# Kernel optimization log

Measured on AMD Instinct MI355X. Metric: run time of the kernel, lower is better.

## Reference

```python
import jax, jax.numpy as jnp
import numpy as np

BH, BW = 64, 64            # base model input (block) size
STRIDE = 16                # block // 4, per WindowObjectDetector.predict
N_CLASSES = 10
THRESH = 0.7


def _extract_patches(x, bh, bw, stride):
    # x: [1, H, W, 3] -> [R, C, bh, bw, 3], VALID padding (tf.image.extract_patches)
    H, W = x.shape[1], x.shape[2]
    R = (H - bh) // stride + 1
    C = (W - bw) // stride + 1
    r = (jnp.arange(R) * stride)[:, None] + jnp.arange(bh)   # [R, bh]
    c = (jnp.arange(C) * stride)[:, None] + jnp.arange(bw)   # [C, bw]
    p = x[0][r]                 # [R, bh, W, 3]
    p = p[:, :, c]              # [R, bh, C, bw, 3]
    return jnp.transpose(p, (0, 2, 1, 3, 4))  # [R, C, bh, bw, 3]


def _connected_components(mask):
    # mask: bool [K, R, C]; 4-connectivity min-label propagation.
    K, R, C = mask.shape
    BIG = jnp.int32(R * C + 2)
    seed = (jnp.arange(R * C, dtype=jnp.int32).reshape(R, C) + 1)[None]  # [1,R,C]
    lbl0 = jnp.where(mask, seed, 0)

    def prop(l):
        xm = jnp.where(mask, l, BIG)
        n = xm
        n = jnp.minimum(n, jnp.pad(xm, ((0, 0), (1, 0), (0, 0)), constant_values=R * C + 2)[:, :R, :])
        n = jnp.minimum(n, jnp.pad(xm, ((0, 0), (0, 1), (0, 0)), constant_values=R * C + 2)[:, 1:, :])
        n = jnp.minimum(n, jnp.pad(xm, ((0, 0), (0, 0), (1, 0)), constant_values=R * C + 2)[:, :, :C])
        n = jnp.minimum(n, jnp.pad(xm, ((0, 0), (0, 0), (0, 1)), constant_values=R * C + 2)[:, :, 1:])
        return jnp.where(mask, n, 0)

    def cond(carry):
        prev, cur = carry
        return jnp.any(prev != cur)

    def body(carry):
        _, cur = carry
        return cur, prop(cur)

    _, lbl = jax.lax.while_loop(cond, body, (lbl0, prop(lbl0)))
    return lbl  # [K, R, C] int32, 0 = background


def _boxes_from_labels(labels):
    # labels: [K, R, C] -> padded boxes [K, R*C+1, 4] (rowmin-1, colmin-1, rowmax+1, colmax+1)
    K, R, C = labels.shape
    S = R * C + 1
    rr = jnp.repeat(jnp.arange(R, dtype=jnp.int32), C)  # [R*C]
    cc = jnp.tile(jnp.arange(C, dtype=jnp.int32), R)
    flat = labels.reshape(K, R * C)

    def per_class(lbl_k):
        rmin = jax.ops.segment_min(rr, lbl_k, num_segments=S)
        rmax = jax.ops.segment_max(rr, lbl_k, num_segments=S)
        cmin = jax.ops.segment_min(cc, lbl_k, num_segments=S)
        cmax = jax.ops.segment_max(cc, lbl_k, num_segments=S)
        cnt = jax.ops.segment_sum(jnp.ones_like(lbl_k), lbl_k, num_segments=S)
        valid = (cnt > 0) & (jnp.arange(S) > 0)
        box = jnp.stack([rmin - 1, cmin - 1, rmax + 1, cmax + 1], axis=-1)
        box = jnp.where(valid[:, None], box, -1)
        return box, valid

    return jax.vmap(per_class)(flat)


def setup_inputs() -> dict:
    key = jax.random.key(0)
    k1, k2, k3 = jax.random.split(key, 3)
    inputs = jax.random.uniform(k1, (1, 1024, 1024, 3), dtype=jnp.float32)
    W = jax.random.normal(k2, (BH * BW * 3, N_CLASSES), dtype=jnp.float32) * 0.02
    b = jax.random.normal(k3, (N_CLASSES,), dtype=jnp.float32)
    return {"inputs": inputs, "W": W, "b": b}


def reference(inputs, W, b):
    # Windowing: extract 64x64 patches with stride 16 (image divisible by 64 -> no resize)
    patches = _extract_patches(inputs, BH, BW, STRIDE)          # [R, C, 64, 64, 3]
    R, C = patches.shape[0], patches.shape[1]
    flat = patches.reshape(R * C, BH * BW * 3)
    logits = flat @ W + b                                        # base model
    prob = jax.nn.softmax(logits, axis=1).reshape(R, C, N_CLASSES)
    mask = prob > THRESH                                         # [R, C, K]
    # tf transposes before/after connected_components (4-connectivity is symmetric)
    labels = _connected_components(jnp.transpose(mask, (2, 0, 1)))  # [K, R, C]
    labels = jnp.transpose(labels, (1, 2, 0))                    # [R, C, K]
    boxes, valid = _boxes_from_labels(jnp.transpose(labels, (2, 0, 1)))
    return prob, labels, boxes, valid
```

## Files before the change

kernel.cpp:

```cpp
#include <hip/hip_runtime.h>
#include <math.h>

#define RG 61
#define CG 61
#define NP 3721
#define NSEG 3722
#define NCLS 10
#define KTOT 12288
#define NPATCH 8
#define KS 2
#define PAIRS_SLICE 3072
#define ITERS 12
#define THRESHV 0.7f
#define BIGI 0x3FFFFFFF

#define DECLBUF(S) float4 wa##S, wb##S, wc##S, wd##S, we##S; \
                   float2 x0##S, x1##S, x2##S, x3##S, x4##S, x5##S, x6##S, x7##S;

#define LOADW(S, IT) { \
    const int e_   = (ksbase + (IT) * 256 + tid) << 1; \
    const int i_   = e_ / 192; \
    const int rem_ = e_ - i_ * 192; \
    const float* wp_ = W + e_ * NCLS;           \
    wa##S = *(const float4*)(wp_); \
    wb##S = *(const float4*)(wp_ + 4); \
    wc##S = *(const float4*)(wp_ + 8); \
    wd##S = *(const float4*)(wp_ + 12); \
    we##S = *(const float4*)(wp_ + 16); \
    const float* xb_ = imgr + i_ * 3072 + rem_; \
    x0##S = *(const float2*)(xb_); \
    x1##S = *(const float2*)(xb_ + 48); \
    x2##S = *(const float2*)(xb_ + 96); \
    x3##S = *(const float2*)(xb_ + 144); \
    x4##S = *(const float2*)(xb_ + 192); \
    x5##S = *(const float2*)(xb_ + 240); \
    x6##S = *(const float2*)(xb_ + 288); \
    x7##S = *(const float2*)(xb_ + 336); \
}

#define FMAS(S) { \
    const float w0_[NCLS] = {wa##S.x, wa##S.y, wa##S.z, wa##S.w, \
                             wb##S.x, wb##S.y, wb##S.z, wb##S.w, wc##S.x, wc##S.y}; \
    const float w1_[NCLS] = {wc##S.z, wc##S.w, wd##S.x, wd##S.y, \
                             wd##S.z, wd##S.w, we##S.x, we##S.y, we##S.z, we##S.w}; \
    const float2 xs_[NPATCH] = {x0##S, x1##S, x2##S, x3##S, x4##S, x5##S, x6##S, x7##S}; \
    _Pragma("unroll") \
    for (int p_ = 0; p_ < NPATCH; ++p_) { \
        _Pragma("unroll") \
        for (int k_ = 0; k_ < NCLS; ++k_) { \
            acc[p_][k_] = fmaf(xs_[p_].x, w0_[k_], acc[p_][k_]); \
            acc[p_][k_] = fmaf(xs_[p_].y, w1_[k_], acc[p_][k_]); \
        } \
    } \
}

#define SBAR() __builtin_amdgcn_sched_barrier(0)

__global__ __launch_bounds__(256, 2) void wod_logits_part(
    const float* __restrict__ img,
    const float* __restrict__ W,
    float* __restrict__ part)
{
    const int tid = threadIdx.x;
    const int blk = blockIdx.x;
    const int ks  = (blk >= 488) ? 1 : 0;
    const int g   = blk - ks * 488;
    const int r   = g >> 3;
    const int cg  = g & 7;
    const int c0  = (cg < 7) ? cg * 8 : 53;

    const int ksbase = ks * PAIRS_SLICE;
    const float* imgr = img + (16 * r) * 3072 + c0 * 48;

    float acc[NPATCH][NCLS];
    #pragma unroll
    for (int p = 0; p < NPATCH; ++p)
        #pragma unroll
        for (int k = 0; k < NCLS; ++k) acc[p][k] = 0.f;

    DECLBUF(A)
    DECLBUF(B)

    LOADW(A, 0)
    #pragma unroll 1
    for (int t = 0; t < ITERS / 2; ++t) {
        SBAR();
        LOADW(B, 2 * t + 1)
        SBAR();
        FMAS(A)
        SBAR();
        if (t < ITERS / 2 - 1) { LOADW(A, 2 * t + 2) }
        SBAR();
        FMAS(B)
        SBAR();
    }

    #pragma unroll
    for (int p = 0; p < NPATCH; ++p)
        #pragma unroll
        for (int k = 0; k < NCLS; ++k) {
            float v = acc[p][k];
            v += __shfl_down(v, 1);
            v += __shfl_down(v, 2);
            v += __shfl_down(v, 4);
            acc[p][k] = v;
        }

    __shared__ float red[32][81];
    const int lane = tid & 63, wave = tid >> 6;
    if ((lane & 7) == 0) {
        const int row = wave * 8 + (lane >> 3);
        #pragma unroll
        for (int p = 0; p < NPATCH; ++p)
            #pragma unroll
            for (int k = 0; k < NCLS; ++k)
                red[row][p * NCLS + k] = acc[p][k];
    }
    __syncthreads();
    if (tid < NPATCH * NCLS) {
        float s = 0.f;
        #pragma unroll
        for (int j = 0; j < 32; ++j) s += red[j][tid];
        part[blk * (NPATCH * NCLS) + tid] = s;
    }
}

__global__ __launch_bounds__(256) void wod_reduce(
    const float* __restrict__ part,
    const float* __restrict__ bias,
    float* __restrict__ out_prob,
    int* __restrict__ mask)
{
    const int cell = blockIdx.x * 256 + threadIdx.x;
    if (cell >= NP) return;
    const int r  = cell / CG;
    const int c  = cell - r * CG;
    int cg = c >> 3; if (cg > 7) cg = 7;
    const int c0 = (cg < 7) ? cg * 8 : 53;
    const int p  = c - c0;
    const int g  = r * 8 + cg;
    const int gb0 = g * (NPATCH * NCLS) + p * NCLS;
    const int gb1 = (488 + g) * (NPATCH * NCLS) + p * NCLS;

    float lg[NCLS];
    #pragma unroll
    for (int k = 0; k < NCLS; ++k)
        lg[k] = bias[k] + part[gb0 + k] + part[gb1 + k];

    float m = -1e30f;
    #pragma unroll
    for (int k = 0; k < NCLS; ++k) m = fmaxf(m, lg[k]);
    float ex[NCLS], s = 0.f;
    #pragma unroll
    for (int k = 0; k < NCLS; ++k) { ex[k] = expf(lg[k] - m); s += ex[k]; }
    const float inv = 1.f / s;
    const int base = cell * NCLS;
    #pragma unroll
    for (int k = 0; k < NCLS; ++k) {
        const float pr = ex[k] * inv;
        out_prob[base + k] = pr;
        mask[k * NP + cell] = (pr > THRESHV) ? 1 : 0;
    }
}

__global__ __launch_bounds__(256) void wod_cc(
    const int* __restrict__ mask,
    float* __restrict__ out_lbl,
    float* __restrict__ out_box,
    float* __restrict__ out_valid)
{
    const int k = blockIdx.x;
    const int tid = threadIdx.x;
    __shared__ int lbl[NP];
    __shared__ int ext0[NSEG], ext1[NSEG];
    __shared__ int changed;

    const int* mk = mask + k * NP;
    for (int idx = tid; idx < NP; idx += 256)
        lbl[idx] = mk[idx] ? (idx + 1) : 0;
    if (tid == 0) changed = 0;
    __syncthreads();

    for (;;) {
        for (int idx = tid; idx < NP; idx += 256) {
            int v = lbl[idx];
            if (v) {
                const int rr = idx / CG;
                const int cc = idx - rr * CG;
                int best = v;
                if (rr > 0)      { int n = lbl[idx - CG]; if (n && n < best) best = n; }
                if (rr < RG - 1) { int n = lbl[idx + CG]; if (n && n < best) best = n; }
                if (cc > 0)      { int n = lbl[idx - 1];  if (n && n < best) best = n; }
                if (cc < CG - 1) { int n = lbl[idx + 1];  if (n && n < best) best = n; }
                if (best < v) { lbl[idx] = best; changed = 1; }
            }
        }
        __syncthreads();
        const bool stop = (changed == 0);
        __syncthreads();
        if (stop) break;
        if (tid == 0) changed = 0;
        __syncthreads();
    }

    for (int idx = tid; idx < NP; idx += 256)
        out_lbl[idx * NCLS + k] = (float)lbl[idx];

    float* boxk = out_box + k * NSEG * 4;
    float* valk = out_valid + k * NSEG;

    for (int s = tid; s < NSEG; s += 256) { ext0[s] = BIGI; ext1[s] = BIGI; }
    __syncthreads();
    for (int idx = tid; idx < NP; idx += 256) {
        const int v = lbl[idx];
        if (v) {
            const int rr = idx / CG, cc = idx - rr * CG;
            atomicMin(&ext0[v], rr);
            atomicMin(&ext1[v], cc);
        }
    }
    __syncthreads();
    for (int s = tid; s < NSEG; s += 256) {
        const bool valid = (s > 0) && (ext0[s] != BIGI);
        boxk[s * 4 + 0] = valid ? (float)(ext0[s] - 1) : -1.f;
        boxk[s * 4 + 1] = valid ? (float)(ext1[s] - 1) : -1.f;
        valk[s] = valid ? 1.f : 0.f;
    }
    __syncthreads();

    for (int s = tid; s < NSEG; s += 256) { ext0[s] = -1; ext1[s] = -1; }
    __syncthreads();
    for (int idx = tid; idx < NP; idx += 256) {
        const int v = lbl[idx];
        if (v) {
            const int rr = idx / CG, cc = idx - rr * CG;
            atomicMax(&ext0[v], rr);
            atomicMax(&ext1[v], cc);
        }
    }
    __syncthreads();
    for (int s = tid; s < NSEG; s += 256) {
        const bool valid = (s > 0) && (ext0[s] >= 0);
        boxk[s * 4 + 2] = valid ? (float)(ext0[s] + 1) : -1.f;
        boxk[s * 4 + 3] = valid ? (float)(ext1[s] + 1) : -1.f;
    }
}

extern "C" void kernel_launch(void* const* d_in, const int* in_sizes, int n_in,
                              void* d_out, int out_size, void* d_ws, size_t ws_size,
                              hipStream_t stream) {
    (void)in_sizes; (void)n_in; (void)out_size; (void)ws_size;
    const float* img = (const float*)d_in[0];
    const float* W   = (const float*)d_in[1];
    const float* b   = (const float*)d_in[2];

    float* out       = (float*)d_out;
    float* out_prob  = out;
    float* out_lbl   = out + 37210;
    float* out_box   = out + 74420;
    float* out_valid = out + 223300;

    int*   mask = (int*)d_ws;
    float* part = (float*)d_ws + NCLS * NP;

    hipLaunchKernelGGL(wod_logits_part, dim3(KS * 488), dim3(256), 0, stream,
                       img, W, part);
    hipLaunchKernelGGL(wod_reduce, dim3((NP + 255) / 256), dim3(256), 0, stream,
                       part, b, out_prob, mask);
    hipLaunchKernelGGL(wod_cc, dim3(NCLS), dim3(256), 0, stream,
                       mask, out_lbl, out_box, out_valid);
}
```

Baseline: 50.96 us.

## Stage image rows in LDS and retile logits GEMM to four patches per block

Each logits block now copies a 32-row by 336-float slab of the image into shared memory once, then reads patch pixels from LDS instead of global memory. Blocks cover four patches instead of eight, which doubles the block count to 1952, and blocks are remapped in an interleaved order; the launch bound is raised to three blocks per SM. The reduce kernel is updated to the new partial-sum layout. This trades more W reloads across blocks and a 43 KB LDS footprint for better parallelism and lower global-memory traffic on the image.

New measurement: 53.56 us. 5.1% more time.

```diff
diff --git a/kernel.cpp b/kernel.cpp
--- a/kernel.cpp
+++ b/kernel.cpp
@@ -6,36 +6,37 @@
 #define NP 3721
 #define NSEG 3722
 #define NCLS 10
-#define KTOT 12288
-#define NPATCH 8
+#define NPATCH 4
+#define NCG 16
 #define KS 2
-#define PAIRS_SLICE 3072
+#define NBLK (RG*NCG*KS)
+#define ROWS_SLICE 32
 #define ITERS 12
+#define IMGF 336
+#define LDSF (ROWS_SLICE*IMGF)
 #define THRESHV 0.7f
 #define BIGI 0x3FFFFFFF
 
+#define SBAR() __builtin_amdgcn_sched_barrier(0)
+
 #define DECLBUF(S) float4 wa##S, wb##S, wc##S, wd##S, we##S; \
-                   float2 x0##S, x1##S, x2##S, x3##S, x4##S, x5##S, x6##S, x7##S;
-
-#define LOADW(S, IT) { \
-    const int e_   = (ksbase + (IT) * 256 + tid) << 1; \
-    const int i_   = e_ / 192; \
-    const int rem_ = e_ - i_ * 192; \
-    const float* wp_ = W + e_ * NCLS;           \
+                   float2 x0##S, x1##S, x2##S, x3##S;
+
+#define LOADAB(S, IT) { \
+    const int pi_  = (IT) * 256 + tid; \
+    const int il_  = pi_ / 96;                \
+    const int rem_ = (pi_ - il_ * 96) * 2;    \
+    const float* wp_ = W + (size_t)((ks * ROWS_SLICE + il_) * 192 + rem_) * NCLS; \
     wa##S = *(const float4*)(wp_); \
     wb##S = *(const float4*)(wp_ + 4); \
     wc##S = *(const float4*)(wp_ + 8); \
     wd##S = *(const float4*)(wp_ + 12); \
     we##S = *(const float4*)(wp_ + 16); \
-    const float* xb_ = imgr + i_ * 3072 + rem_; \
+    const float* xb_ = s + il_ * IMGF + rem_; \
     x0##S = *(const float2*)(xb_); \
     x1##S = *(const float2*)(xb_ + 48); \
     x2##S = *(const float2*)(xb_ + 96); \
     x3##S = *(const float2*)(xb_ + 144); \
-    x4##S = *(const float2*)(xb_ + 192); \
-    x5##S = *(const float2*)(xb_ + 240); \
-    x6##S = *(const float2*)(xb_ + 288); \
-    x7##S = *(const float2*)(xb_ + 336); \
 }
 
 #define FMAS(S) { \
@@ -43,7 +44,7 @@
                              wb##S.x, wb##S.y, wb##S.z, wb##S.w, wc##S.x, wc##S.y}; \
     const float w1_[NCLS] = {wc##S.z, wc##S.w, wd##S.x, wd##S.y, \
                              wd##S.z, wd##S.w, we##S.x, we##S.y, we##S.z, we##S.w}; \
-    const float2 xs_[NPATCH] = {x0##S, x1##S, x2##S, x3##S, x4##S, x5##S, x6##S, x7##S}; \
+    const float2 xs_[NPATCH] = {x0##S, x1##S, x2##S, x3##S}; \
     _Pragma("unroll") \
     for (int p_ = 0; p_ < NPATCH; ++p_) { \
         _Pragma("unroll") \
@@ -54,23 +55,28 @@
     } \
 }
 
-#define SBAR() __builtin_amdgcn_sched_barrier(0)
-
-__global__ __launch_bounds__(256, 2) void wod_logits_part(
+__global__ __launch_bounds__(256, 3) void wod_logits_part(
     const float* __restrict__ img,
     const float* __restrict__ W,
     float* __restrict__ part)
 {
+    __shared__ float s[LDSF];
     const int tid = threadIdx.x;
-    const int blk = blockIdx.x;
-    const int ks  = (blk >= 488) ? 1 : 0;
-    const int g   = blk - ks * 488;
-    const int r   = g >> 3;
-    const int cg  = g & 7;
-    const int c0  = (cg < 7) ? cg * 8 : 53;
-
-    const int ksbase = ks * PAIRS_SLICE;
-    const float* imgr = img + (16 * r) * 3072 + c0 * 48;
+    const int o  = (blockIdx.x & 7) * 244 + (blockIdx.x >> 3);
+    const int r  = o >> 5;
+    const int gg = (o >> 1) & 15;
+    const int ks = o & 1;
+    const int c0 = (gg < 15) ? gg * 4 : 57;
+    const int R0 = 16 * r + ROWS_SLICE * ks;
+
+    const float* gsrc = img + (size_t)R0 * 3072 + c0 * 48;
+    for (int u = tid; u < (LDSF >> 2); u += 256) {
+        const int row  = u / 84;
+        const int col4 = u - row * 84;
+        const float4 v = *(const float4*)(gsrc + row * 3072 + col4 * 4);
+        *(float4*)(s + row * IMGF + col4 * 4) = v;
+    }
+    __syncthreads();
 
     float acc[NPATCH][NCLS];
     #pragma unroll
@@ -81,15 +87,15 @@
     DECLBUF(A)
     DECLBUF(B)
 
-    LOADW(A, 0)
+    LOADAB(A, 0)
     #pragma unroll 1
     for (int t = 0; t < ITERS / 2; ++t) {
         SBAR();
-        LOADW(B, 2 * t + 1)
+        LOADAB(B, 2 * t + 1)
         SBAR();
         FMAS(A)
         SBAR();
-        if (t < ITERS / 2 - 1) { LOADW(A, 2 * t + 2) }
+        if (t < ITERS / 2 - 1) { LOADAB(A, 2 * t + 2) }
         SBAR();
         FMAS(B)
         SBAR();
@@ -106,7 +112,7 @@
             acc[p][k] = v;
         }
 
-    __shared__ float red[32][81];
+    __syncthreads();
     const int lane = tid & 63, wave = tid >> 6;
     if ((lane & 7) == 0) {
         const int row = wave * 8 + (lane >> 3);
@@ -114,14 +120,14 @@
         for (int p = 0; p < NPATCH; ++p)
             #pragma unroll
             for (int k = 0; k < NCLS; ++k)
-                red[row][p * NCLS + k] = acc[p][k];
+                s[row * 40 + p * NCLS + k] = acc[p][k];
     }
     __syncthreads();
     if (tid < NPATCH * NCLS) {
-        float s = 0.f;
-        #pragma unroll
-        for (int j = 0; j < 32; ++j) s += red[j][tid];
-        part[blk * (NPATCH * NCLS) + tid] = s;
+        float sum = 0.f;
+        #pragma unroll
+        for (int j = 0; j < 32; ++j) sum += s[j * 40 + tid];
+        part[o * (NPATCH * NCLS) + tid] = sum;
     }
 }
 
@@ -135,12 +141,12 @@
     if (cell >= NP) return;
     const int r  = cell / CG;
     const int c  = cell - r * CG;
-    int cg = c >> 3; if (cg > 7) cg = 7;
-    const int c0 = (cg < 7) ? cg * 8 : 53;
+    int cg = c >> 2; if (cg > 15) cg = 15;
+    const int c0 = (cg < 15) ? cg * 4 : 57;
     const int p  = c - c0;
-    const int g  = r * 8 + cg;
-    const int gb0 = g * (NPATCH * NCLS) + p * NCLS;
-    const int gb1 = (488 + g) * (NPATCH * NCLS) + p * NCLS;
+    const int o0 = r * 32 + cg * 2;
+    const int gb0 = o0 * (NPATCH * NCLS) + p * NCLS;
+    const int gb1 = (o0 + 1) * (NPATCH * NCLS) + p * NCLS;
 
     float lg[NCLS];
     #pragma unroll
@@ -150,10 +156,10 @@
     float m = -1e30f;
     #pragma unroll
     for (int k = 0; k < NCLS; ++k) m = fmaxf(m, lg[k]);
-    float ex[NCLS], s = 0.f;
-    #pragma unroll
-    for (int k = 0; k < NCLS; ++k) { ex[k] = expf(lg[k] - m); s += ex[k]; }
-    const float inv = 1.f / s;
+    float ex[NCLS], sm = 0.f;
+    #pragma unroll
+    for (int k = 0; k < NCLS; ++k) { ex[k] = expf(lg[k] - m); sm += ex[k]; }
+    const float inv = 1.f / sm;
     const int base = cell * NCLS;
     #pragma unroll
     for (int k = 0; k < NCLS; ++k) {
@@ -209,7 +215,7 @@
     float* boxk = out_box + k * NSEG * 4;
     float* valk = out_valid + k * NSEG;
 
-    for (int s = tid; s < NSEG; s += 256) { ext0[s] = BIGI; ext1[s] = BIGI; }
+    for (int s2 = tid; s2 < NSEG; s2 += 256) { ext0[s2] = BIGI; ext1[s2] = BIGI; }
     __syncthreads();
     for (int idx = tid; idx < NP; idx += 256) {
         const int v = lbl[idx];
@@ -220,15 +226,15 @@
         }
     }
     __syncthreads();
-    for (int s = tid; s < NSEG; s += 256) {
-        const bool valid = (s > 0) && (ext0[s] != BIGI);
-        boxk[s * 4 + 0] = valid ? (float)(ext0[s] - 1) : -1.f;
-        boxk[s * 4 + 1] = valid ? (float)(ext1[s] - 1) : -1.f;
-        valk[s] = valid ? 1.f : 0.f;
-    }
-    __syncthreads();
-
-    for (int s = tid; s < NSEG; s += 256) { ext0[s] = -1; ext1[s] = -1; }
+    for (int s2 = tid; s2 < NSEG; s2 += 256) {
+        const bool valid = (s2 > 0) && (ext0[s2] != BIGI);
+        boxk[s2 * 4 + 0] = valid ? (float)(ext0[s2] - 1) : -1.f;
+        boxk[s2 * 4 + 1] = valid ? (float)(ext1[s2] - 1) : -1.f;
+        valk[s2] = valid ? 1.f : 0.f;
+    }
+    __syncthreads();
+
+    for (int s2 = tid; s2 < NSEG; s2 += 256) { ext0[s2] = -1; ext1[s2] = -1; }
     __syncthreads();
     for (int idx = tid; idx < NP; idx += 256) {
         const int v = lbl[idx];
@@ -239,10 +245,10 @@
         }
     }
     __syncthreads();
-    for (int s = tid; s < NSEG; s += 256) {
-        const bool valid = (s > 0) && (ext0[s] >= 0);
-        boxk[s * 4 + 2] = valid ? (float)(ext0[s] + 1) : -1.f;
-        boxk[s * 4 + 3] = valid ? (float)(ext1[s] + 1) : -1.f;
+    for (int s2 = tid; s2 < NSEG; s2 += 256) {
+        const bool valid = (s2 > 0) && (ext0[s2] >= 0);
+        boxk[s2 * 4 + 2] = valid ? (float)(ext0[s2] + 1) : -1.f;
+        boxk[s2 * 4 + 3] = valid ? (float)(ext1[s2] + 1) : -1.f;
     }
 }
 
@@ -263,7 +269,7 @@
     int*   mask = (int*)d_ws;
     float* part = (float*)d_ws + NCLS * NP;
 
-    hipLaunchKernelGGL(wod_logits_part, dim3(KS * 488), dim3(256), 0, stream,
+    hipLaunchKernelGGL(wod_logits_part, dim3(NBLK), dim3(256), 0, stream,
                        img, W, part);
     hipLaunchKernelGGL(wod_reduce, dim3((NP + 255) / 256), dim3(256), 0, stream,
                        part, b, out_prob, mask);
```
